# Performance work log

Measured on AMD Instinct MI355X. Metric: run time of the kernel, lower is better.

Reference implementation:

```python
import jax, jax.numpy as jnp
import numpy as np

NODE_DIM, HIDDEN, PROJ = 5, 128, 256
NUM_MP = 3
BOX = 1.0


def _knn_edges(positions, k, box_length=BOX):
    """Periodic kNN graph. positions: (B,N,3) -> (src, dst) global flat indices, E = B*N*k."""
    B, N, _ = positions.shape

    def per_batch(pos):  # (N,3)
        delta = jnp.abs(pos[:, None, :] - pos[None, :, :])          # (N,N,3)
        delta = jnp.where(delta > 0.5 * box_length, box_length - delta, delta)
        dist = jnp.sqrt(jnp.sum(delta * delta, axis=-1) + 1e-12)    # (N,N)
        _, idx = jax.lax.top_k(-dist, k + 1)                        # k+1 smallest
        return idx[:, 1:]                                           # drop self -> (N,k)

    nbrs = jax.vmap(per_batch)(positions)                           # (B,N,k)
    offset = (jnp.arange(B) * N)[:, None, None]
    src = jnp.broadcast_to(jnp.arange(N)[None, :, None], (B, N, k)) + offset
    dst = nbrs + offset
    return src.reshape(-1), dst.reshape(-1)


def setup_inputs() -> dict:
    key = jax.random.key(0)
    ks = jax.random.split(key, 16)
    B, N = 8, 2048
    s = 0.05
    inp = {
        "x": jax.random.normal(ks[0], (B, N, NODE_DIM), jnp.float32),
        "positions": jax.random.uniform(ks[1], (B, N, 3), jnp.float32),
        "k": 16,
        # encoder: Linear(5,128)+ReLU, Linear(128,128)+ReLU
        "enc_w0": jax.random.normal(ks[2], (NODE_DIM, HIDDEN), jnp.float32) * s,
        "enc_b0": jnp.zeros((HIDDEN,), jnp.float32),
        "enc_w1": jax.random.normal(ks[3], (HIDDEN, HIDDEN), jnp.float32) * s,
        "enc_b1": jnp.zeros((HIDDEN,), jnp.float32),
        # message nets: Linear(2H,H)+ReLU per round
        "msg_w": jax.random.normal(ks[4], (NUM_MP, 2 * HIDDEN, HIDDEN), jnp.float32) * s,
        "msg_b": jnp.zeros((NUM_MP, HIDDEN), jnp.float32),
        # update nets: Linear(2H,H)+ReLU per round
        "upd_w": jax.random.normal(ks[5], (NUM_MP, 2 * HIDDEN, HIDDEN), jnp.float32) * s,
        "upd_b": jnp.zeros((NUM_MP, HIDDEN), jnp.float32),
        # projection head: Linear(H,H)+ReLU, Linear(H,proj)
        "proj_w0": jax.random.normal(ks[6], (HIDDEN, HIDDEN), jnp.float32) * s,
        "proj_b0": jnp.zeros((HIDDEN,), jnp.float32),
        "proj_w1": jax.random.normal(ks[7], (HIDDEN, PROJ), jnp.float32) * s,
        "proj_b1": jnp.zeros((PROJ,), jnp.float32),
    }
    return inp


def reference(x, positions, k, enc_w0, enc_b0, enc_w1, enc_b1,
              msg_w, msg_b, upd_w, upd_b, proj_w0, proj_b0, proj_w1, proj_b1):
    B, N, _ = x.shape
    BN = B * N
    relu = jax.nn.relu

    # encoder over flattened nodes
    h = relu(x.reshape(BN, -1) @ enc_w0 + enc_b0)
    h = relu(h @ enc_w1 + enc_b1)

    src, dst = _knn_edges(positions, k)
    E = src.shape[0]
    deg = jax.ops.segment_sum(jnp.ones((E,), h.dtype), dst, num_segments=BN)
    inv_deg = 1.0 / jnp.clip(deg, 1.0)

    for i in range(NUM_MP):
        # per-edge message: concat(sender, receiver) -> Linear+ReLU
        msg = relu(jnp.concatenate([h[src], h[dst]], axis=-1) @ msg_w[i] + msg_b[i])
        # mean aggregation at destination nodes
        agg = jax.ops.segment_sum(msg, dst, num_segments=BN) * inv_deg[:, None]
        # residual update
        h = h + relu(jnp.concatenate([h, agg], axis=-1) @ upd_w[i] + upd_b[i])

    z = relu(h @ proj_w0 + proj_b0) @ proj_w1 + proj_b1
    return z.reshape(B, N, PROJ), h.reshape(B, N, HIDDEN)
```

## Files before the change

### kernel.cpp

```cpp
#include <hip/hip_runtime.h>
#include <stdint.h>
#include <math.h>

#define NN 2048
#define BB 8
#define BN (BB*NN)
#define KK 16
#define EE (BN*KK)
#define HID 128
#define PROJ_D 256
#define QPB 16

typedef unsigned long long u64;
typedef unsigned short ushort_t;
typedef __attribute__((ext_vector_type(8))) short short8;
typedef __attribute__((ext_vector_type(4))) float f32x4;

__device__ __forceinline__ u64 wave_min_u64(u64 v) {
  #pragma unroll
  for (int off = 32; off > 0; off >>= 1) {
    u64 o = __shfl_xor(v, off);
    v = o < v ? o : v;
  }
  return v;
}

__global__ __launch_bounds__(1024) void knn_kernel(const float* __restrict__ pos,
                                                   int* __restrict__ nbr,
                                                   int* __restrict__ cnt) {
  __shared__ float4 Ps[NN];
  __shared__ unsigned Hist[QPB * 256];
  const int b  = blockIdx.x >> 7;
  const int qb = blockIdx.x & 127;
  const int wave = threadIdx.x >> 6;
  const int lane = threadIdx.x & 63;
  const int i = qb * QPB + wave;
  const float* P = pos + (size_t)b * NN * 3;

  for (int t = threadIdx.x; t < NN; t += 1024)
    Ps[t] = make_float4(P[t*3], P[t*3+1], P[t*3+2], 0.f);
  __syncthreads();

  const float4 pi = Ps[i];
  const float xi = pi.x, yi = pi.y, zi = pi.z;
  unsigned* H = &Hist[wave * 256];

  float d[32];
  #pragma unroll
  for (int t = 0; t < 32; t++) {
    int j = t * 64 + lane;
    float4 pj = Ps[j];
    float tx = xi - pj.x, ty = yi - pj.y, tz = zi - pj.z;
    float dx = __fsub_rn(tx, rintf(tx));
    float dy = __fsub_rn(ty, rintf(ty));
    float dz = __fsub_rn(tz, rintf(tz));
    float s = __fadd_rn(__fadd_rn(__fadd_rn(__fmul_rn(dx,dx), __fmul_rn(dy,dy)),
                                  __fmul_rn(dz,dz)), 1e-12f);
    d[t] = __fsqrt_rn(s);
  }

  float scale = 1024.0f;
  int bstar = 0; unsigned C = 0;
  for (;;) {
    *(uint4*)&H[lane * 4] = make_uint4(0u, 0u, 0u, 0u);
    #pragma unroll
    for (int t = 0; t < 32; t++) {
      int bin = (int)(d[t] * scale);
      if (bin < 256) atomicAdd(&H[bin], 1u);
    }
    uint4 cv = *(const uint4*)&H[lane * 4];
    unsigned s4 = cv.x + cv.y + cv.z + cv.w;
    unsigned incl = s4;
    #pragma unroll
    for (int off = 1; off < 64; off <<= 1) {
      unsigned v = __shfl_up(incl, off);
      if (lane >= off) incl += v;
    }
    unsigned total = __shfl(incl, 63);
    if (total >= 17u) {
      unsigned base = incl - s4;
      bool has = (incl >= 17u) && (base < 17u);
      u64 hmask = __ballot(has);
      int srcl = __ffsll((unsigned long long)hmask) - 1;
      int bl = 0; unsigned Cl = 0;
      if (has) {
        if (base + cv.x >= 17u)                    { bl = lane*4 + 0; Cl = base; }
        else if (base + cv.x + cv.y >= 17u)        { bl = lane*4 + 1; Cl = base + cv.x; }
        else if (base + cv.x + cv.y + cv.z >= 17u) { bl = lane*4 + 2; Cl = base + cv.x + cv.y; }
        else                                       { bl = lane*4 + 3; Cl = base + cv.x + cv.y + cv.z; }
      }
      bstar = __shfl(bl, srcl);
      C     = __shfl(Cl, srcl);
      break;
    }
    scale *= 0.25f;
  }
  const int m = 17 - (int)C;

  u64 lst[6];
  #pragma unroll
  for (int t = 0; t < 6; t++) lst[t] = ~0ull;
  #pragma unroll
  for (int t = 0; t < 32; t++) {
    int bin = (int)(d[t] * scale);
    u64 key = ((u64)__float_as_uint(d[t]) << 11) | (unsigned)(t * 64 + lane);
    u64 cand = (bin == bstar) ? key : ~0ull;
    if (cand < lst[5]) {
      lst[5] = cand;
      #pragma unroll
      for (int u = 5; u > 0; u--) {
        u64 a = lst[u-1], c2 = lst[u];
        lst[u-1] = a < c2 ? a : c2;
        lst[u]   = a < c2 ? c2 : a;
      }
    }
  }

  u64 kstar = 0;
  #pragma unroll 1
  for (int r = 0; r < m; r++) {
    u64 h0 = lst[0];
    u64 gm = wave_min_u64(h0);
    kstar = gm;
    bool win = (h0 == gm);
    #pragma unroll
    for (int u = 0; u < 5; u++) lst[u] = win ? lst[u+1] : lst[u];
    lst[5] = win ? ~0ull : lst[5];
  }

  int* outp = nbr + ((size_t)b * NN + i) * KK;
  int total = 0;
  #pragma unroll
  for (int t = 0; t < 32; t++) {
    int j = t * 64 + lane;
    u64 key = ((u64)__float_as_uint(d[t]) << 11) | (unsigned)j;
    bool pred = (key <= kstar) && (j != i);
    u64 msk = __ballot(pred);
    if (pred) {
      int ofs = total + __popcll(msk & ((1ull << lane) - 1ull));
      outp[ofs] = b * NN + j;
      atomicAdd(&cnt[b * NN + j], 1);
    }
    total += __popcll(msk);
  }
}

__global__ __launch_bounds__(256) void scan_kernel(const int* __restrict__ cnt,
                                                   int* __restrict__ row_ptr) {
  __shared__ int ps[256];
  int t = threadIdx.x;
  const int4* cv = (const int4*)(cnt + t * 64);
  int4 c[16];
  int s = 0;
  #pragma unroll
  for (int i = 0; i < 16; i++) {
    c[i] = cv[i];
    s += c[i].x + c[i].y + c[i].z + c[i].w;
  }
  ps[t] = s;
  __syncthreads();
  for (int off = 1; off < 256; off <<= 1) {
    int v = 0;
    if (t >= off) v = ps[t - off];
    __syncthreads();
    ps[t] += v;
    __syncthreads();
  }
  int run = t ? ps[t - 1] : 0;
  int4* rp = (int4*)(row_ptr + t * 64);
  #pragma unroll
  for (int i = 0; i < 16; i++) {
    int4 o;
    o.x = run; run += c[i].x;
    o.y = run; run += c[i].y;
    o.z = run; run += c[i].z;
    o.w = run; run += c[i].w;
    rp[i] = o;
  }
  if (t == 255) row_ptr[BN] = run;
}

__global__ __launch_bounds__(256) void fill_kernel(const int* __restrict__ nbr,
                                                   const int* __restrict__ row_ptr,
                                                   int* __restrict__ fill,
                                                   int* __restrict__ col) {
  int e = blockIdx.x * 256 + threadIdx.x;
  int d = nbr[e];
  int srcn = e >> 4;
  int p = row_ptr[d] + atomicAdd(&fill[d], 1);
  col[p] = srcn;
}

__global__ __launch_bounds__(256) void enc0_kernel(const float* __restrict__ x,
                                                   const float* __restrict__ w0,
                                                   const float* __restrict__ b0,
                                                   float* __restrict__ h) {
  int t = blockIdx.x * 256 + threadIdx.x;
  int m = t >> 5;
  int c = (t & 31) * 4;
  float xv[5];
  #pragma unroll
  for (int d = 0; d < 5; d++) xv[d] = x[m * 5 + d];
  float4 acc = *(const float4*)&b0[c];
  #pragma unroll
  for (int d = 0; d < 5; d++) {
    float4 w = *(const float4*)&w0[d * HID + c];
    acc.x += xv[d] * w.x; acc.y += xv[d] * w.y;
    acc.z += xv[d] * w.z; acc.w += xv[d] * w.w;
  }
  acc.x = fmaxf(acc.x, 0.f); acc.y = fmaxf(acc.y, 0.f);
  acc.z = fmaxf(acc.z, 0.f); acc.w = fmaxf(acc.w, 0.f);
  *(float4*)&h[(size_t)m * HID + c] = acc;
}

__device__ __forceinline__ unsigned cvtpk_bf16(float a, float b) {
  unsigned r;
  asm("v_cvt_pk_bf16_f32 %0, %1, %2" : "=v"(r) : "v"(a), "v"(b));
  return r;
}

__device__ __forceinline__ void cvt8(const float4 f0, const float4 f1,
                                     short8& hi, short8& lo) {
  unsigned h0 = cvtpk_bf16(f0.x, f0.y);
  unsigned h1 = cvtpk_bf16(f0.z, f0.w);
  unsigned h2 = cvtpk_bf16(f1.x, f1.y);
  unsigned h3 = cvtpk_bf16(f1.z, f1.w);
  unsigned l0 = cvtpk_bf16(f0.x - __uint_as_float(h0 << 16),
                           f0.y - __uint_as_float(h0 & 0xffff0000u));
  unsigned l1 = cvtpk_bf16(f0.z - __uint_as_float(h1 << 16),
                           f0.w - __uint_as_float(h1 & 0xffff0000u));
  unsigned l2 = cvtpk_bf16(f1.x - __uint_as_float(h2 << 16),
                           f1.y - __uint_as_float(h2 & 0xffff0000u));
  unsigned l3 = cvtpk_bf16(f1.z - __uint_as_float(h3 << 16),
                           f1.w - __uint_as_float(h3 & 0xffff0000u));
  union { unsigned u[4]; short8 v; } H, L;
  H.u[0] = h0; H.u[1] = h1; H.u[2] = h2; H.u[3] = h3;
  L.u[0] = l0; L.u[1] = l1; L.u[2] = l2; L.u[3] = l3;
  hi = H.v;
  lo = L.v;
}

__global__ __launch_bounds__(256) void prep_w_kernel(
    const float* __restrict__ enc_w1, const float* __restrict__ msg_w,
    const float* __restrict__ upd_w, const float* __restrict__ proj_w0,
    const float* __restrict__ proj_w1, ushort_t* __restrict__ wfrag) {
  int u = blockIdx.x >> 3;
  int c = (blockIdx.x & 7) * 256 + threadIdx.x;
  const float* src;
  int ldW = HID;
  if (u == 0) src = enc_w1;
  else if (u <= 6)  { int i = (u-1)>>1; int hf = (u-1)&1; src = msg_w + ((size_t)i*256 + hf*128) * HID; }
  else if (u <= 12) { int i = (u-7)>>1; int hf = (u-7)&1; src = upd_w + ((size_t)i*256 + hf*128) * HID; }
  else if (u == 13) src = proj_w0;
  else { src = proj_w1 + (u - 14) * 128; ldW = PROJ_D; }

  int ks = c >> 9, ct = (c >> 6) & 7, lane = c & 63;
  int colc = ct * 16 + (lane & 15);
  int k0 = ks * 32 + ((lane >> 4) << 3);
  float f[8];
  #pragma unroll
  for (int e = 0; e < 8; e++) f[e] = src[(size_t)(k0 + e) * ldW + colc];
  short8 hv, lv;
  cvt8(make_float4(f[0],f[1],f[2],f[3]), make_float4(f[4],f[5],f[6],f[7]), hv, lv);
  *(short8*)&wfrag[(size_t)u * 32768 + (size_t)c * 8] = hv;
  *(short8*)&wfrag[(size_t)u * 32768 + 16384 + (size_t)c * 8] = lv;
}

__device__ __forceinline__ void stage_A_convert(ushort_t* Ahi, ushort_t* Alo,
                                                const float* A, int m0, int tid) {
  #pragma unroll
  for (int i = 0; i < 4; i++) {
    int c = tid + i * 256;
    int row = c >> 4, kg = c & 15;
    const float4* ap = (const float4*)(A + (((size_t)m0 + row) << 7) + (kg << 3));
    short8 hv, lv;
    cvt8(ap[0], ap[1], hv, lv);
    int idx = (((row >> 4) * 4 + (kg >> 2)) * 64 + ((row & 15) | ((kg & 3) << 4))) * 8;
    *(short8*)&Ahi[idx] = hv;
    *(short8*)&Alo[idx] = lv;
  }
}

__device__ __forceinline__ void unit_mfma(f32x4 acc[8], const ushort_t* wf,
                                          const ushort_t* Ahi, const ushort_t* Alo,
                                          ushort_t* Bhi, ushort_t* Blo,
                                          int tid, int lane, int wid) {
  #pragma unroll 1
  for (int half = 0; half < 2; half++) {
    __syncthreads();
    const short8* ghi = (const short8*)(wf + half * 8192);
    const short8* glo = (const short8*)(wf + 16384 + half * 8192);
    #pragma unroll
    for (int i = 0; i < 4; i++) {
      ((short8*)Bhi)[tid + i * 256] = ghi[tid + i * 256];
      ((short8*)Blo)[tid + i * 256] = glo[tid + i * 256];
    }
    __syncthreads();
    #pragma unroll
    for (int ks2 = 0; ks2 < 2; ks2++) {
      int ksA = half * 2 + ks2;
      short8 ah = *(const short8*)&Ahi[((wid * 4 + ksA) * 64 + lane) * 8];
      short8 al = *(const short8*)&Alo[((wid * 4 + ksA) * 64 + lane) * 8];
      #pragma unroll
      for (int ct = 0; ct < 8; ct++) {
        short8 bh = *(const short8*)&Bhi[((ks2 * 8 + ct) * 64 + lane) * 8];
        short8 bl = *(const short8*)&Blo[((ks2 * 8 + ct) * 64 + lane) * 8];
        acc[ct] = __builtin_amdgcn_mfma_f32_16x16x32_bf16(ah, bh, acc[ct], 0, 0, 0);
        acc[ct] = __builtin_amdgcn_mfma_f32_16x16x32_bf16(ah, bl, acc[ct], 0, 0, 0);
        acc[ct] = __builtin_amdgcn_mfma_f32_16x16x32_bf16(al, bh, acc[ct], 0, 0, 0);
      }
    }
  }
}

__device__ __forceinline__ void unit_mfma_h(f32x4 acc[4], const ushort_t* wf,
                                            int ct0,
                                            const ushort_t* Ahi, const ushort_t* Alo,
                                            ushort_t* Bhi, ushort_t* Blo,
                                            int tid, int lane, int wid) {
  #pragma unroll 1
  for (int half = 0; half < 2; half++) {
    __syncthreads();
    #pragma unroll
    for (int i = 0; i < 2; i++) {
      int sc = tid + i * 256;
      int ks2 = sc >> 8;
      int cts = (sc >> 6) & 3;
      int ln  = sc & 63;
      int c = half * 1024 + ks2 * 512 + (ct0 + cts) * 64 + ln;
      ((short8*)Bhi)[sc] = *(const short8*)&wf[(size_t)c * 8];
      ((short8*)Blo)[sc] = *(const short8*)&wf[16384 + (size_t)c * 8];
    }
    __syncthreads();
    #pragma unroll
    for (int ks2 = 0; ks2 < 2; ks2++) {
      int ksA = half * 2 + ks2;
      short8 ah = *(const short8*)&Ahi[((wid * 4 + ksA) * 64 + lane) * 8];
      short8 al = *(const short8*)&Alo[((wid * 4 + ksA) * 64 + lane) * 8];
      #pragma unroll
      for (int ct = 0; ct < 4; ct++) {
        short8 bh = *(const short8*)&Bhi[((ks2 * 4 + ct) * 64 + lane) * 8];
        short8 bl = *(const short8*)&Blo[((ks2 * 4 + ct) * 64 + lane) * 8];
        acc[ct] = __builtin_amdgcn_mfma_f32_16x16x32_bf16(ah, bh, acc[ct], 0, 0, 0);
        acc[ct] = __builtin_amdgcn_mfma_f32_16x16x32_bf16(ah, bl, acc[ct], 0, 0, 0);
        acc[ct] = __builtin_amdgcn_mfma_f32_16x16x32_bf16(al, bh, acc[ct], 0, 0, 0);
      }
    }
  }
}

template<int RELU>
__global__ __launch_bounds__(256, 4) void g1_kernel(
    const float* __restrict__ A, const ushort_t* __restrict__ wf,
    const float* __restrict__ bias, float* __restrict__ out) {
  __shared__ ushort_t Ahi[8192], Alo[8192], Bhi[4096], Blo[4096];
  const int tid = threadIdx.x, lane = tid & 63, wid = tid >> 6;
  const int m0 = blockIdx.x * 64, ct0 = blockIdx.y * 4;
  stage_A_convert(Ahi, Alo, A, m0, tid);
  f32x4 acc[4];
  f32x4 z = {0.f, 0.f, 0.f, 0.f};
  #pragma unroll
  for (int ct = 0; ct < 4; ct++) acc[ct] = z;
  unit_mfma_h(acc, wf, ct0, Ahi, Alo, Bhi, Blo, tid, lane, wid);

  const int rbase = m0 + wid * 16 + ((lane >> 4) << 2);
  const int cb = lane & 15;
  #pragma unroll
  for (int ct = 0; ct < 4; ct++) {
    int n = (ct0 + ct) * 16 + cb;
    float bv = bias ? bias[n] : 0.f;
    #pragma unroll
    for (int r = 0; r < 4; r++) {
      float v = acc[ct][r] + bv;
      if (RELU) v = fmaxf(v, 0.f);
      out[(size_t)(rbase + r) * HID + n] = v;
    }
  }
}

__global__ __launch_bounds__(256, 4) void msg_kernel(
    const float* __restrict__ h, const ushort_t* __restrict__ wfT,
    const ushort_t* __restrict__ wfB, const float* __restrict__ mb,
    float* __restrict__ bufA, float* __restrict__ bufB) {
  __shared__ ushort_t Ahi[8192], Alo[8192], Bhi[8192], Blo[8192];
  const int tid = threadIdx.x, lane = tid & 63, wid = tid >> 6;
  const int m0 = blockIdx.x * 64;
  const int y = blockIdx.y;
  stage_A_convert(Ahi, Alo, h, m0, tid);
  f32x4 acc[8];
  f32x4 z = {0.f, 0.f, 0.f, 0.f};
  #pragma unroll
  for (int ct = 0; ct < 8; ct++) acc[ct] = z;
  unit_mfma(acc, y ? wfB : wfT, Ahi, Alo, Bhi, Blo, tid, lane, wid);

  float* out = y ? bufB : bufA;
  const float* bias = y ? mb : nullptr;
  const int rbase = m0 + wid * 16 + ((lane >> 4) << 2);
  const int cb = lane & 15;
  #pragma unroll
  for (int ct = 0; ct < 8; ct++) {
    int n = ct * 16 + cb;
    float bv = bias ? bias[n] : 0.f;
    #pragma unroll
    for (int r = 0; r < 4; r++)
      out[(size_t)(rbase + r) * HID + n] = acc[ct][r] + bv;
  }
}

__global__ __launch_bounds__(256, 4) void upd_kernel(
    const float* __restrict__ h, const ushort_t* __restrict__ wuT,
    const float* __restrict__ aggF, const ushort_t* __restrict__ wuB,
    const float* __restrict__ ub, float* __restrict__ out) {
  __shared__ ushort_t Ahi[8192], Alo[8192], Bhi[4096], Blo[4096];
  const int tid = threadIdx.x, lane = tid & 63, wid = tid >> 6;
  const int m0 = blockIdx.x * 64, ct0 = blockIdx.y * 4;
  stage_A_convert(Ahi, Alo, h, m0, tid);
  f32x4 acc[4];
  f32x4 z = {0.f, 0.f, 0.f, 0.f};
  #pragma unroll
  for (int ct = 0; ct < 4; ct++) acc[ct] = z;
  unit_mfma_h(acc, wuT, ct0, Ahi, Alo, Bhi, Blo, tid, lane, wid);
  __syncthreads();
  stage_A_convert(Ahi, Alo, aggF, m0, tid);
  unit_mfma_h(acc, wuB, ct0, Ahi, Alo, Bhi, Blo, tid, lane, wid);

  const int rbase = m0 + wid * 16 + ((lane >> 4) << 2);
  const int cb = lane & 15;
  #pragma unroll
  for (int ct = 0; ct < 4; ct++) {
    int n = (ct0 + ct) * 16 + cb;
    float bv = ub[n];
    #pragma unroll
    for (int r = 0; r < 4; r++) {
      float v = fmaxf(acc[ct][r] + bv, 0.f)
              + h[(size_t)(rbase + r) * HID + n];
      out[(size_t)(rbase + r) * HID + n] = v;
    }
  }
}

__global__ __launch_bounds__(256, 4) void proj1_kernel(
    const float* __restrict__ A, const ushort_t* __restrict__ wf01,
    const float* __restrict__ pb1, float* __restrict__ zout) {
  __shared__ ushort_t Ahi[8192], Alo[8192], Bhi[8192], Blo[8192];
  const int tid = threadIdx.x, lane = tid & 63, wid = tid >> 6;
  const int m0 = blockIdx.x * 64;
  const int y = blockIdx.y;
  stage_A_convert(Ahi, Alo, A, m0, tid);
  f32x4 acc[8];
  f32x4 z = {0.f, 0.f, 0.f, 0.f};
  #pragma unroll
  for (int ct = 0; ct < 8; ct++) acc[ct] = z;
  unit_mfma(acc, wf01 + (size_t)y * 32768, Ahi, Alo, Bhi, Blo, tid, lane, wid);

  const int rbase = m0 + wid * 16 + ((lane >> 4) << 2);
  const int cb = lane & 15;
  #pragma unroll
  for (int ct = 0; ct < 8; ct++) {
    int n = y * 128 + ct * 16 + cb;
    float bv = pb1[n];
    #pragma unroll
    for (int r = 0; r < 4; r++)
      zout[(size_t)(rbase + r) * PROJ_D + n] = acc[ct][r] + bv;
  }
}

__global__ __launch_bounds__(256) void agg_kernel(const float* __restrict__ Abuf,
                                                  const float* __restrict__ Bbuf,
                                                  const int* __restrict__ row_ptr,
                                                  const int* __restrict__ col,
                                                  float* __restrict__ agg) {
  int j = blockIdx.x * 2 + (threadIdx.x >> 7);
  int c = threadIdx.x & 127;
  float bj = Bbuf[(size_t)j * HID + c];
  int s = row_ptr[j], e = row_ptr[j + 1];
  float acc = 0.f;
  int p = s;
  for (; p + 4 <= e; p += 4) {
    int i0 = col[p], i1 = col[p+1], i2 = col[p+2], i3 = col[p+3];
    float v0 = Abuf[(size_t)i0 * HID + c];
    float v1 = Abuf[(size_t)i1 * HID + c];
    float v2 = Abuf[(size_t)i2 * HID + c];
    float v3 = Abuf[(size_t)i3 * HID + c];
    acc += fmaxf(v0 + bj, 0.f) + fmaxf(v1 + bj, 0.f)
         + fmaxf(v2 + bj, 0.f) + fmaxf(v3 + bj, 0.f);
  }
  for (; p < e; p++) {
    int i = col[p];
    acc += fmaxf(Abuf[(size_t)i * HID + c] + bj, 0.f);
  }
  float deg = (float)(e - s);
  float inv = 1.0f / fmaxf(deg, 1.0f);
  agg[(size_t)j * HID + c] = acc * inv;
}

extern "C" void kernel_launch(void* const* d_in, const int* in_sizes, int n_in,
                              void* d_out, int out_size, void* d_ws, size_t ws_size,
                              hipStream_t stream) {
  (void)in_sizes; (void)n_in; (void)out_size; (void)ws_size;
  const float* x       = (const float*)d_in[0];
  const float* pos     = (const float*)d_in[1];
  const float* enc_w0  = (const float*)d_in[3];
  const float* enc_b0  = (const float*)d_in[4];
  const float* enc_w1  = (const float*)d_in[5];
  const float* enc_b1  = (const float*)d_in[6];
  const float* msg_w   = (const float*)d_in[7];
  const float* msg_b   = (const float*)d_in[8];
  const float* upd_w   = (const float*)d_in[9];
  const float* upd_b   = (const float*)d_in[10];
  const float* proj_w0 = (const float*)d_in[11];
  const float* proj_b0 = (const float*)d_in[12];
  const float* proj_w1 = (const float*)d_in[13];
  const float* proj_b1 = (const float*)d_in[14];

  char* ws = (char*)d_ws;
  size_t off = 0;
  auto alloc = [&](size_t bytes) -> void* {
    void* p = ws + off;
    off += (bytes + 255) & ~(size_t)255;
    return p;
  };
  int*      nbr     = (int*)alloc((size_t)EE * 4);
  int*      cnt     = (int*)alloc((size_t)BN * 4);
  int*      fill    = (int*)alloc((size_t)BN * 4);
  int*      row_ptr = (int*)alloc((size_t)(BN + 1) * 4);
  int*      col     = (int*)alloc((size_t)EE * 4);
  float*    h_a     = (float*)alloc((size_t)BN * HID * 4);
  float*    h_b     = (float*)alloc((size_t)BN * HID * 4);
  float*    bufA    = (float*)alloc((size_t)BN * HID * 4);
  float*    bufB    = (float*)alloc((size_t)BN * HID * 4);
  float*    bufAgg  = (float*)alloc((size_t)BN * HID * 4);
  ushort_t* wfrag   = (ushort_t*)alloc((size_t)16 * 32768 * 2);
  float*    out     = (float*)d_out;
  float*    hOut    = out + (size_t)BN * PROJ_D;

  hipMemsetAsync(cnt, 0, (size_t)BN * 4 * 2, stream);

  prep_w_kernel<<<128, 256, 0, stream>>>(enc_w1, msg_w, upd_w, proj_w0, proj_w1, wfrag);
  knn_kernel<<<BN / QPB, 1024, 0, stream>>>(pos, nbr, cnt);
  scan_kernel<<<1, 256, 0, stream>>>(cnt, row_ptr);
  fill_kernel<<<EE / 256, 256, 0, stream>>>(nbr, row_ptr, fill, col);

  enc0_kernel<<<BN * 32 / 256, 256, 0, stream>>>(x, enc_w0, enc_b0, bufA);
  g1_kernel<1><<<dim3(BN / 64, 2), 256, 0, stream>>>(bufA, wfrag + 0 * 32768,
                                                     enc_b1, h_a);

  float* hc = h_a;
  float* hn = h_b;
  for (int i = 0; i < 3; i++) {
    msg_kernel<<<dim3(BN / 64, 2), 256, 0, stream>>>(
        hc, wfrag + (size_t)(1 + 2 * i) * 32768,
        wfrag + (size_t)(2 + 2 * i) * 32768, msg_b + (size_t)i * HID,
        bufA, bufB);
    agg_kernel<<<BN / 2, 256, 0, stream>>>(bufA, bufB, row_ptr, col, bufAgg);
    float* target = (i == 2) ? hOut : hn;
    upd_kernel<<<dim3(BN / 64, 2), 256, 0, stream>>>(
        hc, wfrag + (size_t)(7 + 2 * i) * 32768, bufAgg,
        wfrag + (size_t)(8 + 2 * i) * 32768, upd_b + (size_t)i * HID, target);
    hn = hc; hc = target;
  }

  g1_kernel<1><<<dim3(BN / 64, 2), 256, 0, stream>>>(hc, wfrag + 13 * 32768,
                                                     proj_b0, bufA);
  proj1_kernel<<<dim3(BN / 64, 2), 256, 0, stream>>>(
      bufA, wfrag + 14 * 32768, proj_b1, out);
}
```

Before: 243.0 us.

## Use spatial cell grid to prune kNN candidates to neighboring cells

```diff
diff --git a/kernel.cpp b/kernel.cpp
--- a/kernel.cpp
+++ b/kernel.cpp
@@ -10,6 +10,9 @@
 #define HID 128
 #define PROJ_D 256
 #define QPB 16
+#define CDIM 6
+#define NCELL (CDIM*CDIM*CDIM)
+#define CAP 768
 
 typedef unsigned long long u64;
 typedef unsigned short ushort_t;
@@ -25,48 +28,124 @@
   return v;
 }
 
-__global__ __launch_bounds__(1024) void knn_kernel(const float* __restrict__ pos,
-                                                   int* __restrict__ nbr,
-                                                   int* __restrict__ cnt) {
+__global__ __launch_bounds__(256) void cellsort_kernel(
+    const float* __restrict__ pos, float4* __restrict__ spos,
+    int* __restrict__ cptr) {
+  __shared__ int hist[NCELL];
+  __shared__ int base[NCELL];
+  const int b = blockIdx.x, tid = threadIdx.x;
+  if (tid < NCELL) hist[tid] = 0;
+  __syncthreads();
+  int cellv[8];
+  float4 pv[8];
+  #pragma unroll
+  for (int k = 0; k < 8; k++) {
+    int j = tid * 8 + k;
+    const float* pp = pos + ((size_t)b * NN + j) * 3;
+    float x = pp[0], y = pp[1], z = pp[2];
+    int cx = (int)(x * 6.0f); cx = cx > 5 ? 5 : cx;
+    int cy = (int)(y * 6.0f); cy = cy > 5 ? 5 : cy;
+    int cz = (int)(z * 6.0f); cz = cz > 5 ? 5 : cz;
+    int cell = (cx * 6 + cy) * 6 + cz;
+    cellv[k] = cell;
+    pv[k] = make_float4(x, y, z, __int_as_float(j));
+    atomicAdd(&hist[cell], 1);
+  }
+  __syncthreads();
+  if (tid == 0) {
+    int run = 0;
+    for (int c = 0; c < NCELL; c++) {
+      cptr[b * (NCELL + 1) + c] = run;
+      base[c] = run;
+      run += hist[c];
+    }
+    cptr[b * (NCELL + 1) + NCELL] = run;
+  }
+  __syncthreads();
+  if (tid < NCELL) hist[tid] = 0;
+  __syncthreads();
+  #pragma unroll
+  for (int k = 0; k < 8; k++) {
+    int slot = base[cellv[k]] + atomicAdd(&hist[cellv[k]], 1);
+    spos[(size_t)b * NN + slot] = pv[k];
+  }
+}
+
+__global__ __launch_bounds__(1024) void knn_kernel(
+    const float4* __restrict__ spos, const int* __restrict__ cptr,
+    int* __restrict__ nbr, int* __restrict__ cnt) {
   __shared__ float4 Ps[NN];
   __shared__ unsigned Hist[QPB * 256];
+  __shared__ ushort_t Cand[QPB * CAP];
+  __shared__ int Cp[NCELL + 1];
   const int b  = blockIdx.x >> 7;
   const int qb = blockIdx.x & 127;
   const int wave = threadIdx.x >> 6;
   const int lane = threadIdx.x & 63;
-  const int i = qb * QPB + wave;
-  const float* P = pos + (size_t)b * NN * 3;
+  const int s_q = qb * QPB + wave;
 
   for (int t = threadIdx.x; t < NN; t += 1024)
-    Ps[t] = make_float4(P[t*3], P[t*3+1], P[t*3+2], 0.f);
+    Ps[t] = spos[(size_t)b * NN + t];
+  if (threadIdx.x <= NCELL)
+    Cp[threadIdx.x] = cptr[b * (NCELL + 1) + threadIdx.x];
   __syncthreads();
 
-  const float4 pi = Ps[i];
-  const float xi = pi.x, yi = pi.y, zi = pi.z;
+  const float4 q = Ps[s_q];
+  const float xi = q.x, yi = q.y, zi = q.z;
+  const int orig_i = __float_as_int(q.w);
   unsigned* H = &Hist[wave * 256];
-
-  float d[32];
-  #pragma unroll
-  for (int t = 0; t < 32; t++) {
-    int j = t * 64 + lane;
-    float4 pj = Ps[j];
-    float tx = xi - pj.x, ty = yi - pj.y, tz = zi - pj.z;
-    float dx = __fsub_rn(tx, rintf(tx));
-    float dy = __fsub_rn(ty, rintf(ty));
-    float dz = __fsub_rn(tz, rintf(tz));
-    float s = __fadd_rn(__fadd_rn(__fadd_rn(__fmul_rn(dx,dx), __fmul_rn(dy,dy)),
-                                  __fmul_rn(dz,dz)), 1e-12f);
-    d[t] = __fsqrt_rn(s);
-  }
-
-  float scale = 1024.0f;
+  ushort_t* CL = &Cand[wave * CAP];
+
+  int cx = (int)(xi * 6.0f); cx = cx > 5 ? 5 : cx;
+  int cy = (int)(yi * 6.0f); cy = cy > 5 ? 5 : cy;
+  int cz = (int)(zi * 6.0f); cz = cz > 5 ? 5 : cz;
+
+  int T = 0;
+  bool ovf = false;
+  #pragma unroll 1
+  for (int dxy = 0; dxy < 9; dxy++) {
+    int dx = dxy / 3 - 1, dy = dxy - (dxy / 3) * 3 - 1;
+    int ncx = cx + dx; ncx += (ncx < 0) ? 6 : 0; ncx -= (ncx >= 6) ? 6 : 0;
+    int ncy = cy + dy; ncy += (ncy < 0) ? 6 : 0; ncy -= (ncy >= 6) ? 6 : 0;
+    int cbse = (ncx * 6 + ncy) * 6;
+    int s0, l0, s1 = 0, l1 = 0;
+    if (cz == 0) {
+      s0 = Cp[cbse + 5]; l0 = Cp[cbse + 6] - s0;
+      s1 = Cp[cbse];     l1 = Cp[cbse + 2] - s1;
+    } else if (cz == 5) {
+      s0 = Cp[cbse + 4]; l0 = Cp[cbse + 6] - s0;
+      s1 = Cp[cbse];     l1 = Cp[cbse + 1] - s1;
+    } else {
+      s0 = Cp[cbse + cz - 1]; l0 = Cp[cbse + cz + 2] - s0;
+    }
+    if (T + l0 + l1 > CAP) { ovf = true; break; }
+    for (int t = lane; t < l0; t += 64) CL[T + t] = (ushort_t)(s0 + t);
+    T += l0;
+    for (int t = lane; t < l1; t += 64) CL[T + t] = (ushort_t)(s1 + t);
+    T += l1;
+  }
+
+  int mode = ovf ? 1 : 0;
+  float scale = 1536.0f;
+  int T2 = T, binmax = 254;
   int bstar = 0; unsigned C = 0;
   for (;;) {
+    scale = mode ? 256.0f : 1536.0f;
+    T2 = mode ? NN : T;
+    binmax = mode ? 256 : 254;
     *(uint4*)&H[lane * 4] = make_uint4(0u, 0u, 0u, 0u);
-    #pragma unroll
-    for (int t = 0; t < 32; t++) {
-      int bin = (int)(d[t] * scale);
-      if (bin < 256) atomicAdd(&H[bin], 1u);
+    for (int t = lane; t < T2; t += 64) {
+      int p = mode ? t : (int)CL[t];
+      float4 pj = Ps[p];
+      float tx = xi - pj.x, ty = yi - pj.y, tz = zi - pj.z;
+      float ddx = __fsub_rn(tx, rintf(tx));
+      float ddy = __fsub_rn(ty, rintf(ty));
+      float ddz = __fsub_rn(tz, rintf(tz));
+      float s = __fadd_rn(__fadd_rn(__fadd_rn(__fmul_rn(ddx,ddx), __fmul_rn(ddy,ddy)),
+                                    __fmul_rn(ddz,ddz)), 1e-12f);
+      float d = __fsqrt_rn(s);
+      int bin = (int)(d * scale);
+      if (bin < binmax) atomicAdd(&H[bin], 1u);
     }
     uint4 cv = *(const uint4*)&H[lane * 4];
     unsigned s4 = cv.x + cv.y + cv.z + cv.w;
@@ -93,25 +172,34 @@
       C     = __shfl(Cl, srcl);
       break;
     }
-    scale *= 0.25f;
+    mode = 1;
   }
   const int m = 17 - (int)C;
 
   u64 lst[6];
   #pragma unroll
   for (int t = 0; t < 6; t++) lst[t] = ~0ull;
-  #pragma unroll
-  for (int t = 0; t < 32; t++) {
-    int bin = (int)(d[t] * scale);
-    u64 key = ((u64)__float_as_uint(d[t]) << 11) | (unsigned)(t * 64 + lane);
-    u64 cand = (bin == bstar) ? key : ~0ull;
-    if (cand < lst[5]) {
-      lst[5] = cand;
-      #pragma unroll
-      for (int u = 5; u > 0; u--) {
-        u64 a = lst[u-1], c2 = lst[u];
-        lst[u-1] = a < c2 ? a : c2;
-        lst[u]   = a < c2 ? c2 : a;
+  for (int t = lane; t < T2; t += 64) {
+    int p = mode ? t : (int)CL[t];
+    float4 pj = Ps[p];
+    float tx = xi - pj.x, ty = yi - pj.y, tz = zi - pj.z;
+    float ddx = __fsub_rn(tx, rintf(tx));
+    float ddy = __fsub_rn(ty, rintf(ty));
+    float ddz = __fsub_rn(tz, rintf(tz));
+    float s = __fadd_rn(__fadd_rn(__fadd_rn(__fmul_rn(ddx,ddx), __fmul_rn(ddy,ddy)),
+                                  __fmul_rn(ddz,ddz)), 1e-12f);
+    float d = __fsqrt_rn(s);
+    int bin = (int)(d * scale);
+    if (bin == bstar) {
+      u64 key = ((u64)__float_as_uint(d) << 11) | (unsigned)__float_as_int(pj.w);
+      if (key < lst[5]) {
+        lst[5] = key;
+        #pragma unroll
+        for (int u = 5; u > 0; u--) {
+          u64 a = lst[u-1], c2 = lst[u];
+          lst[u-1] = a < c2 ? a : c2;
+          lst[u]   = a < c2 ? c2 : a;
+        }
       }
     }
   }
@@ -128,20 +216,33 @@
     lst[5] = win ? ~0ull : lst[5];
   }
 
-  int* outp = nbr + ((size_t)b * NN + i) * KK;
-  int total = 0;
-  #pragma unroll
-  for (int t = 0; t < 32; t++) {
-    int j = t * 64 + lane;
-    u64 key = ((u64)__float_as_uint(d[t]) << 11) | (unsigned)j;
-    bool pred = (key <= kstar) && (j != i);
+  int* outp = nbr + ((size_t)b * NN + orig_i) * KK;
+  int total_e = 0;
+  for (int t0 = 0; t0 < T2; t0 += 64) {
+    int t = t0 + lane;
+    bool pred = false;
+    int oj = 0;
+    if (t < T2) {
+      int p = mode ? t : (int)CL[t];
+      float4 pj = Ps[p];
+      float tx = xi - pj.x, ty = yi - pj.y, tz = zi - pj.z;
+      float ddx = __fsub_rn(tx, rintf(tx));
+      float ddy = __fsub_rn(ty, rintf(ty));
+      float ddz = __fsub_rn(tz, rintf(tz));
+      float s = __fadd_rn(__fadd_rn(__fadd_rn(__fmul_rn(ddx,ddx), __fmul_rn(ddy,ddy)),
+                                    __fmul_rn(ddz,ddz)), 1e-12f);
+      float d = __fsqrt_rn(s);
+      oj = __float_as_int(pj.w);
+      u64 key = ((u64)__float_as_uint(d) << 11) | (unsigned)oj;
+      pred = (key <= kstar) && (oj != orig_i);
+    }
     u64 msk = __ballot(pred);
     if (pred) {
-      int ofs = total + __popcll(msk & ((1ull << lane) - 1ull));
-      outp[ofs] = b * NN + j;
-      atomicAdd(&cnt[b * NN + j], 1);
-    }
-    total += __popcll(msk);
+      int ofs = total_e + __popcll(msk & ((1ull << lane) - 1ull));
+      outp[ofs] = b * NN + oj;
+      atomicAdd(&cnt[b * NN + oj], 1);
+    }
+    total_e += __popcll(msk);
   }
 }
 
@@ -531,13 +632,16 @@
   float*    bufB    = (float*)alloc((size_t)BN * HID * 4);
   float*    bufAgg  = (float*)alloc((size_t)BN * HID * 4);
   ushort_t* wfrag   = (ushort_t*)alloc((size_t)16 * 32768 * 2);
+  float4*   spos    = (float4*)alloc((size_t)BN * 16);
+  int*      cptr    = (int*)alloc((size_t)BB * (NCELL + 1) * 4);
   float*    out     = (float*)d_out;
   float*    hOut    = out + (size_t)BN * PROJ_D;
 
   hipMemsetAsync(cnt, 0, (size_t)BN * 4 * 2, stream);
 
+  cellsort_kernel<<<BB, 256, 0, stream>>>(pos, spos, cptr);
   prep_w_kernel<<<128, 256, 0, stream>>>(enc_w1, msg_w, upd_w, proj_w0, proj_w1, wfrag);
-  knn_kernel<<<BN / QPB, 1024, 0, stream>>>(pos, nbr, cnt);
+  knn_kernel<<<BN / QPB, 1024, 0, stream>>>(spos, cptr, nbr, cnt);
   scan_kernel<<<1, 256, 0, stream>>>(cnt, row_ptr);
   fill_kernel<<<EE / 256, 256, 0, stream>>>(nbr, row_ptr, fill, col);
 
```

New measurement: 229.0 us. 5.8% less time.
